# Performance work log

Measured on AMD Instinct MI355X. Metric: run time of the kernel, lower is better.

The kernel has to match this reference:

```python
import jax, jax.numpy as jnp
import numpy as np
from jax import lax

CIN, COUT = 128, 256
BN_EPS = 1e-5


def setup_inputs() -> dict:
    key = jax.random.key(0)
    ks = jax.random.split(key, 12)
    B, E, T = 4, 256, 128
    sc_in = 1.0 / np.sqrt(CIN)
    sc_out = 1.0 / np.sqrt(COUT)
    return {
        "x_e": jax.random.normal(ks[0], (B, E, T, CIN), dtype=jnp.float32),
        "Wp": jax.random.uniform(ks[1], (COUT, CIN), minval=-sc_in, maxval=sc_in, dtype=jnp.float32),
        "bp": jax.random.uniform(ks[2], (COUT,), minval=-sc_in, maxval=sc_in, dtype=jnp.float32),
        "a_param": jax.random.normal(ks[3], (COUT,), dtype=jnp.float32) * 0.1,
        "Wb": jax.random.uniform(ks[4], (COUT, COUT), minval=-sc_out, maxval=sc_out, dtype=jnp.float32),
        "bb": jax.random.uniform(ks[5], (COUT,), minval=-sc_out, maxval=sc_out, dtype=jnp.float32),
        "Wg": jax.random.uniform(ks[6], (COUT, COUT), minval=-sc_out, maxval=sc_out, dtype=jnp.float32),
        "bg": jax.random.uniform(ks[7], (COUT,), minval=-sc_out, maxval=sc_out, dtype=jnp.float32),
        "Wd": jax.random.uniform(ks[8], (COUT, COUT), minval=-sc_out, maxval=sc_out, dtype=jnp.float32),
        "bd": jax.random.uniform(ks[9], (COUT,), minval=-sc_out, maxval=sc_out, dtype=jnp.float32),
        "gamma": jnp.ones((COUT,), dtype=jnp.float32),
        "beta": jnp.zeros((COUT,), dtype=jnp.float32),
        "run_mean": jnp.zeros((COUT,), dtype=jnp.float32),
        "run_var": jnp.ones((COUT,), dtype=jnp.float32),
    }


def reference(x_e, Wp, bp, a_param, Wb, bb, Wg, bg, Wd, bd, gamma, beta, run_mean, run_var):
    # 1x1 conv over channel dim == pointwise linear: [B,E,T,Ci] @ [Co,Ci]^T
    x = jnp.einsum('betc,oc->beto', x_e, Wp) + bp              # [B,E,T,C]
    a = jnp.tanh(a_param)                                       # [C] per-channel decay
    u = jnp.einsum('betc,oc->beto', x, Wb) + bb                 # [B,E,T,C]

    # linear recurrence s_t = a * s_{t-1} + u_t, s_{-1} = 0 (scan over T)
    u_t = jnp.moveaxis(u, 2, 0)                                 # [T,B,E,C]

    def step(s, ut):
        s = a * s + ut
        return s, s

    s0 = jnp.zeros(u_t.shape[1:], dtype=u.dtype)
    _, S = lax.scan(step, s0, u_t)                              # [T,B,E,C]
    S = jnp.moveaxis(S, 0, 2)                                   # [B,E,T,C]

    # output projection applied to all timesteps at once
    y = (jnp.einsum('betc,oc->beto', S, Wg) + bg
         + jnp.einsum('betc,oc->beto', x, Wd) + bd)

    # BatchNorm2d (eval mode: running stats), channel-last layout
    y = (y - run_mean) * lax.rsqrt(run_var + BN_EPS) * gamma + beta
    y = jax.nn.gelu(y, approximate=False)
    return y + x  # dropout is identity in eval
```

## Files before the change

kernel.cpp:

```cpp
#include <hip/hip_runtime.h>
#include <hip/hip_bf16.h>

#define T 128
#define CIN 128
#define C 256
#define NBE 1024

typedef short bf8_t __attribute__((ext_vector_type(8)));
typedef float f4_t __attribute__((ext_vector_type(4)));

__device__ inline short f2bf(float f) {
  union { float f; unsigned u; } v; v.f = f;
  unsigned r = v.u + 0x7FFFu + ((v.u >> 16) & 1u);
  return (short)(r >> 16);
}
__device__ inline float bf2f(short s) {
  union { unsigned u; float f; } v; v.u = ((unsigned)(unsigned short)s) << 16;
  return v.f;
}
__device__ inline f4_t mfma16(bf8_t a, bf8_t b, f4_t c) {
  return __builtin_amdgcn_mfma_f32_16x16x32_bf16(a, b, c, 0, 0, 0);
}
__device__ inline bf8_t lds_frag(const short* base, int row, int kcol, int rowc) {
  return *reinterpret_cast<const bf8_t*>(base + row * rowc + (kcol ^ ((row & 7) << 3)));
}

__global__ void prep_weights(const float* __restrict__ Wp, const float* __restrict__ Wb,
                             const float* __restrict__ Wg, const float* __restrict__ Wd,
                             short* __restrict__ ws) {
  int i = blockIdx.x * 256 + threadIdx.x;
  if (i < 32768) ws[i] = f2bf(Wp[i]);
  ws[32768 + i]  = f2bf(Wb[i]);
  ws[98304 + i]  = f2bf(Wg[i]);
  ws[163840 + i] = f2bf(Wd[i]);
}

__global__ __launch_bounds__(512, 1) void fused_ssm(
    const float* __restrict__ xe, const short* __restrict__ wgt,
    const float* __restrict__ bp, const float* __restrict__ a_param,
    const float* __restrict__ bb, const float* __restrict__ bg,
    const float* __restrict__ bd, const float* __restrict__ gamma,
    const float* __restrict__ beta, const float* __restrict__ rmean,
    const float* __restrict__ rvar, float* __restrict__ out) {
  __shared__ __align__(16) short lds_x[T * C];
  __shared__ __align__(16) short lds_u[T * C];
  short* lds_xe = lds_u;

  const int tid = threadIdx.x;
  const int lane = tid & 63;
  const int w = tid >> 6;
  const int wr = w >> 1;
  const int wc = w & 1;
  const int l15 = lane & 15;
  const int l4 = lane >> 4;
  const int be = blockIdx.x;

  const float* xe_blk = xe + (size_t)be * T * CIN;
  float* out_blk = out + (size_t)be * T * C;

  const short* Wpb = wgt;
  const short* Wbb = wgt + 32768;
  const short* Wgb = wgt + 98304;
  const short* Wdb = wgt + 163840;

#pragma unroll
  for (int j = 0; j < 32; ++j) {
    int idx = j * 512 + tid;
    int r = idx >> 7, c = idx & 127;
    lds_xe[r * 128 + (c ^ ((r & 7) << 3))] = f2bf(xe_blk[idx]);
  }
  __syncthreads();

  const int row_a0 = wr * 32 + l15;
  const int col0 = wc * 128 + l15;

  f4_t acc[2][8];

#pragma unroll
  for (int mi = 0; mi < 2; ++mi)
#pragma unroll
    for (int ni = 0; ni < 8; ++ni) acc[mi][ni] = (f4_t)(0.f);

#pragma unroll
  for (int kk = 0; kk < 4; ++kk) {
    int kcol = kk * 32 + l4 * 8;
    bf8_t a0 = lds_frag(lds_xe, row_a0, kcol, 128);
    bf8_t a1 = lds_frag(lds_xe, row_a0 + 16, kcol, 128);
#pragma unroll
    for (int ni = 0; ni < 8; ++ni) {
      bf8_t b = *reinterpret_cast<const bf8_t*>(Wpb + (col0 + ni * 16) * 128 + kcol);
      acc[0][ni] = mfma16(a0, b, acc[0][ni]);
      acc[1][ni] = mfma16(a1, b, acc[1][ni]);
    }
  }
#pragma unroll
  for (int ni = 0; ni < 8; ++ni) {
    int col = col0 + ni * 16;
    float bias = bp[col];
#pragma unroll
    for (int mi = 0; mi < 2; ++mi)
#pragma unroll
      for (int r = 0; r < 4; ++r) {
        int row = wr * 32 + mi * 16 + l4 * 4 + r;
        lds_x[row * 256 + (col ^ ((row & 7) << 3))] = f2bf(acc[mi][ni][r] + bias);
      }
  }
  __syncthreads();

#pragma unroll
  for (int mi = 0; mi < 2; ++mi)
#pragma unroll
    for (int ni = 0; ni < 8; ++ni) acc[mi][ni] = (f4_t)(0.f);

#pragma unroll
  for (int kk = 0; kk < 8; ++kk) {
    int kcol = kk * 32 + l4 * 8;
    bf8_t a0 = lds_frag(lds_x, row_a0, kcol, 256);
    bf8_t a1 = lds_frag(lds_x, row_a0 + 16, kcol, 256);
#pragma unroll
    for (int ni = 0; ni < 8; ++ni) {
      bf8_t b = *reinterpret_cast<const bf8_t*>(Wbb + (col0 + ni * 16) * 256 + kcol);
      acc[0][ni] = mfma16(a0, b, acc[0][ni]);
      acc[1][ni] = mfma16(a1, b, acc[1][ni]);
    }
  }
#pragma unroll
  for (int ni = 0; ni < 8; ++ni) {
    int col = col0 + ni * 16;
    float bias = bb[col];
#pragma unroll
    for (int mi = 0; mi < 2; ++mi)
#pragma unroll
      for (int r = 0; r < 4; ++r) {
        int row = wr * 32 + mi * 16 + l4 * 4 + r;
        lds_u[row * 256 + (col ^ ((row & 7) << 3))] = f2bf(acc[mi][ni][r] + bias);
      }
  }
  __syncthreads();

  if (tid < 256) {
    float a = tanhf(a_param[tid]);
    float s = 0.f;
    for (int t = 0; t < T; ++t) {
      int idx = t * 256 + (tid ^ ((t & 7) << 3));
      s = a * s + bf2f(lds_u[idx]);
      lds_u[idx] = f2bf(s);
    }
  }
  __syncthreads();

#pragma unroll
  for (int mi = 0; mi < 2; ++mi)
#pragma unroll
    for (int ni = 0; ni < 8; ++ni) acc[mi][ni] = (f4_t)(0.f);

#pragma unroll
  for (int kk = 0; kk < 8; ++kk) {
    int kcol = kk * 32 + l4 * 8;
    bf8_t s0 = lds_frag(lds_u, row_a0, kcol, 256);
    bf8_t s1 = lds_frag(lds_u, row_a0 + 16, kcol, 256);
    bf8_t x0 = lds_frag(lds_x, row_a0, kcol, 256);
    bf8_t x1 = lds_frag(lds_x, row_a0 + 16, kcol, 256);
#pragma unroll
    for (int ni = 0; ni < 8; ++ni) {
      bf8_t bgf = *reinterpret_cast<const bf8_t*>(Wgb + (col0 + ni * 16) * 256 + kcol);
      acc[0][ni] = mfma16(s0, bgf, acc[0][ni]);
      acc[1][ni] = mfma16(s1, bgf, acc[1][ni]);
      bf8_t bdf = *reinterpret_cast<const bf8_t*>(Wdb + (col0 + ni * 16) * 256 + kcol);
      acc[0][ni] = mfma16(x0, bdf, acc[0][ni]);
      acc[1][ni] = mfma16(x1, bdf, acc[1][ni]);
    }
  }

#pragma unroll
  for (int ni = 0; ni < 8; ++ni) {
    int col = col0 + ni * 16;
    float bsum = bg[col] + bd[col];
    float mu = rmean[col];
    float rstd = rsqrtf(rvar[col] + 1e-5f);
    float ga = gamma[col], bt = beta[col];
#pragma unroll
    for (int mi = 0; mi < 2; ++mi)
#pragma unroll
      for (int r = 0; r < 4; ++r) {
        int row = wr * 32 + mi * 16 + l4 * 4 + r;
        float y = acc[mi][ni][r] + bsum;
        y = (y - mu) * rstd * ga + bt;
        float g = 0.5f * y * (1.f + erff(y * 0.70710678118654752f));
        float xv = bf2f(lds_x[row * 256 + (col ^ ((row & 7) << 3))]);
        out_blk[row * 256 + col] = g + xv;
      }
  }
}

extern "C" void kernel_launch(void* const* d_in, const int* in_sizes, int n_in,
                              void* d_out, int out_size, void* d_ws, size_t ws_size,
                              hipStream_t stream) {
  const float* xe    = (const float*)d_in[0];
  const float* Wp    = (const float*)d_in[1];
  const float* bp    = (const float*)d_in[2];
  const float* ap    = (const float*)d_in[3];
  const float* Wb    = (const float*)d_in[4];
  const float* bb    = (const float*)d_in[5];
  const float* Wg    = (const float*)d_in[6];
  const float* bg    = (const float*)d_in[7];
  const float* Wd    = (const float*)d_in[8];
  const float* bd    = (const float*)d_in[9];
  const float* gamma = (const float*)d_in[10];
  const float* beta  = (const float*)d_in[11];
  const float* rmean = (const float*)d_in[12];
  const float* rvar  = (const float*)d_in[13];
  float* out = (float*)d_out;
  short* wgt = (short*)d_ws;

  prep_weights<<<256, 256, 0, stream>>>(Wp, Wb, Wg, Wd, wgt);
  fused_ssm<<<NBE, 512, 0, stream>>>(xe, wgt, bp, ap, bb, bg, bd, gamma, beta,
                                     rmean, rvar, out);
}
```

Before: 298.0 us.

## Use 1024-thread blocks, vectorize input loads, and stage output through LDS

After: 376.4 us. +26.3%, slower.

```diff
diff --git a/kernel.cpp b/kernel.cpp
--- a/kernel.cpp
+++ b/kernel.cpp
@@ -7,6 +7,7 @@
 #define NBE 1024
 
 typedef short bf8_t __attribute__((ext_vector_type(8)));
+typedef short s4_t __attribute__((ext_vector_type(4)));
 typedef float f4_t __attribute__((ext_vector_type(4)));
 
 __device__ inline short f2bf(float f) {
@@ -35,22 +36,21 @@
   ws[163840 + i] = f2bf(Wd[i]);
 }
 
-__global__ __launch_bounds__(512, 1) void fused_ssm(
+__global__ __launch_bounds__(1024) void fused_ssm(
     const float* __restrict__ xe, const short* __restrict__ wgt,
     const float* __restrict__ bp, const float* __restrict__ a_param,
     const float* __restrict__ bb, const float* __restrict__ bg,
     const float* __restrict__ bd, const float* __restrict__ gamma,
     const float* __restrict__ beta, const float* __restrict__ rmean,
     const float* __restrict__ rvar, float* __restrict__ out) {
-  __shared__ __align__(16) short lds_x[T * C];
-  __shared__ __align__(16) short lds_u[T * C];
-  short* lds_xe = lds_u;
+  __shared__ __align__(16) short lds[2][T * C];
+  float* fbuf = reinterpret_cast<float*>(lds);
 
   const int tid = threadIdx.x;
   const int lane = tid & 63;
   const int w = tid >> 6;
-  const int wr = w >> 1;
-  const int wc = w & 1;
+  const int wr = w >> 2;
+  const int wcg = w & 3;
   const int l15 = lane & 15;
   const int l4 = lane >> 4;
   const int be = blockIdx.x;
@@ -63,46 +63,54 @@
   const short* Wgb = wgt + 98304;
   const short* Wdb = wgt + 163840;
 
-#pragma unroll
-  for (int j = 0; j < 32; ++j) {
-    int idx = j * 512 + tid;
-    int r = idx >> 7, c = idx & 127;
-    lds_xe[r * 128 + (c ^ ((r & 7) << 3))] = f2bf(xe_blk[idx]);
+  {
+    const float4* xe4 = reinterpret_cast<const float4*>(xe_blk);
+#pragma unroll
+    for (int j = 0; j < 4; ++j) {
+      float4 v = xe4[j * 1024 + tid];
+      int fi = j * 4096 + tid * 4;
+      int r = fi >> 7, c = fi & 127;
+      s4_t p = {f2bf(v.x), f2bf(v.y), f2bf(v.z), f2bf(v.w)};
+      *reinterpret_cast<s4_t*>(&lds[1][r * 128 + (c ^ ((r & 7) << 3))]) = p;
+    }
   }
   __syncthreads();
 
   const int row_a0 = wr * 32 + l15;
-  const int col0 = wc * 128 + l15;
-
-  f4_t acc[2][8];
+  const int colbase = wcg * 64 + l15;
+
+  f4_t acc[2][4];
 
 #pragma unroll
   for (int mi = 0; mi < 2; ++mi)
 #pragma unroll
-    for (int ni = 0; ni < 8; ++ni) acc[mi][ni] = (f4_t)(0.f);
+    for (int ni = 0; ni < 4; ++ni) acc[mi][ni] = (f4_t)(0.f);
 
 #pragma unroll
   for (int kk = 0; kk < 4; ++kk) {
     int kcol = kk * 32 + l4 * 8;
-    bf8_t a0 = lds_frag(lds_xe, row_a0, kcol, 128);
-    bf8_t a1 = lds_frag(lds_xe, row_a0 + 16, kcol, 128);
-#pragma unroll
-    for (int ni = 0; ni < 8; ++ni) {
-      bf8_t b = *reinterpret_cast<const bf8_t*>(Wpb + (col0 + ni * 16) * 128 + kcol);
-      acc[0][ni] = mfma16(a0, b, acc[0][ni]);
-      acc[1][ni] = mfma16(a1, b, acc[1][ni]);
-    }
-  }
-#pragma unroll
-  for (int ni = 0; ni < 8; ++ni) {
-    int col = col0 + ni * 16;
+    bf8_t a0 = lds_frag(lds[1], row_a0, kcol, 128);
+    bf8_t a1 = lds_frag(lds[1], row_a0 + 16, kcol, 128);
+    bf8_t bfr[4];
+#pragma unroll
+    for (int ni = 0; ni < 4; ++ni)
+      bfr[ni] = *reinterpret_cast<const bf8_t*>(Wpb + (colbase + ni * 16) * 128 + kcol);
+#pragma unroll
+    for (int ni = 0; ni < 4; ++ni) {
+      acc[0][ni] = mfma16(a0, bfr[ni], acc[0][ni]);
+      acc[1][ni] = mfma16(a1, bfr[ni], acc[1][ni]);
+    }
+  }
+#pragma unroll
+  for (int ni = 0; ni < 4; ++ni) {
+    int col = colbase + ni * 16;
     float bias = bp[col];
 #pragma unroll
     for (int mi = 0; mi < 2; ++mi)
 #pragma unroll
       for (int r = 0; r < 4; ++r) {
         int row = wr * 32 + mi * 16 + l4 * 4 + r;
-        lds_x[row * 256 + (col ^ ((row & 7) << 3))] = f2bf(acc[mi][ni][r] + bias);
+        lds[0][row * 256 + (col ^ ((row & 7) << 3))] = f2bf(acc[mi][ni][r] + bias);
       }
   }
   __syncthreads();
@@ -110,30 +118,33 @@
 #pragma unroll
   for (int mi = 0; mi < 2; ++mi)
 #pragma unroll
-    for (int ni = 0; ni < 8; ++ni) acc[mi][ni] = (f4_t)(0.f);
+    for (int ni = 0; ni < 4; ++ni) acc[mi][ni] = (f4_t)(0.f);
 
 #pragma unroll
   for (int kk = 0; kk < 8; ++kk) {
     int kcol = kk * 32 + l4 * 8;
-    bf8_t a0 = lds_frag(lds_x, row_a0, kcol, 256);
-    bf8_t a1 = lds_frag(lds_x, row_a0 + 16, kcol, 256);
-#pragma unroll
-    for (int ni = 0; ni < 8; ++ni) {
-      bf8_t b = *reinterpret_cast<const bf8_t*>(Wbb + (col0 + ni * 16) * 256 + kcol);
-      acc[0][ni] = mfma16(a0, b, acc[0][ni]);
-      acc[1][ni] = mfma16(a1, b, acc[1][ni]);
-    }
-  }
-#pragma unroll
-  for (int ni = 0; ni < 8; ++ni) {
-    int col = col0 + ni * 16;
+    bf8_t a0 = lds_frag(lds[0], row_a0, kcol, 256);
+    bf8_t a1 = lds_frag(lds[0], row_a0 + 16, kcol, 256);
+    bf8_t bfr[4];
+#pragma unroll
+    for (int ni = 0; ni < 4; ++ni)
+      bfr[ni] = *reinterpret_cast<const bf8_t*>(Wbb + (colbase + ni * 16) * 256 + kcol);
+#pragma unroll
+    for (int ni = 0; ni < 4; ++ni) {
+      acc[0][ni] = mfma16(a0, bfr[ni], acc[0][ni]);
+      acc[1][ni] = mfma16(a1, bfr[ni], acc[1][ni]);
+    }
+  }
+#pragma unroll
+  for (int ni = 0; ni < 4; ++ni) {
+    int col = colbase + ni * 16;
     float bias = bb[col];
 #pragma unroll
     for (int mi = 0; mi < 2; ++mi)
 #pragma unroll
       for (int r = 0; r < 4; ++r) {
         int row = wr * 32 + mi * 16 + l4 * 4 + r;
-        lds_u[row * 256 + (col ^ ((row & 7) << 3))] = f2bf(acc[mi][ni][r] + bias);
+        lds[1][row * 256 + (col ^ ((row & 7) << 3))] = f2bf(acc[mi][ni][r] + bias);
       }
   }
   __syncthreads();
@@ -141,10 +152,13 @@
   if (tid < 256) {
     float a = tanhf(a_param[tid]);
     float s = 0.f;
-    for (int t = 0; t < T; ++t) {
-      int idx = t * 256 + (tid ^ ((t & 7) << 3));
-      s = a * s + bf2f(lds_u[idx]);
-      lds_u[idx] = f2bf(s);
+    float un = bf2f(lds[1][tid]);
+#pragma unroll 8
+    for (int t = 0; t < 128; ++t) {
+      float unn = (t < 127) ? bf2f(lds[1][(t + 1) * 256 + (tid ^ (((t + 1) & 7) << 3))]) : 0.f;
+      s = a * s + un;
+      lds[1][t * 256 + (tid ^ ((t & 7) << 3))] = f2bf(s);
+      un = unn;
     }
   }
   __syncthreads();
@@ -152,29 +166,33 @@
 #pragma unroll
   for (int mi = 0; mi < 2; ++mi)
 #pragma unroll
-    for (int ni = 0; ni < 8; ++ni) acc[mi][ni] = (f4_t)(0.f);
+    for (int ni = 0; ni < 4; ++ni) acc[mi][ni] = (f4_t)(0.f);
 
 #pragma unroll
   for (int kk = 0; kk < 8; ++kk) {
     int kcol = kk * 32 + l4 * 8;
-    bf8_t s0 = lds_frag(lds_u, row_a0, kcol, 256);
-    bf8_t s1 = lds_frag(lds_u, row_a0 + 16, kcol, 256);
-    bf8_t x0 = lds_frag(lds_x, row_a0, kcol, 256);
-    bf8_t x1 = lds_frag(lds_x, row_a0 + 16, kcol, 256);
-#pragma unroll
-    for (int ni = 0; ni < 8; ++ni) {
-      bf8_t bgf = *reinterpret_cast<const bf8_t*>(Wgb + (col0 + ni * 16) * 256 + kcol);
-      acc[0][ni] = mfma16(s0, bgf, acc[0][ni]);
-      acc[1][ni] = mfma16(s1, bgf, acc[1][ni]);
-      bf8_t bdf = *reinterpret_cast<const bf8_t*>(Wdb + (col0 + ni * 16) * 256 + kcol);
-      acc[0][ni] = mfma16(x0, bdf, acc[0][ni]);
-      acc[1][ni] = mfma16(x1, bdf, acc[1][ni]);
-    }
-  }
-
-#pragma unroll
-  for (int ni = 0; ni < 8; ++ni) {
-    int col = col0 + ni * 16;
+    bf8_t s0 = lds_frag(lds[1], row_a0, kcol, 256);
+    bf8_t s1 = lds_frag(lds[1], row_a0 + 16, kcol, 256);
+    bf8_t x0 = lds_frag(lds[0], row_a0, kcol, 256);
+    bf8_t x1 = lds_frag(lds[0], row_a0 + 16, kcol, 256);
+    bf8_t bgf[4], bdf[4];
+#pragma unroll
+    for (int ni = 0; ni < 4; ++ni) {
+      bgf[ni] = *reinterpret_cast<const bf8_t*>(Wgb + (colbase + ni * 16) * 256 + kcol);
+      bdf[ni] = *reinterpret_cast<const bf8_t*>(Wdb + (colbase + ni * 16) * 256 + kcol);
+    }
+#pragma unroll
+    for (int ni = 0; ni < 4; ++ni) {
+      acc[0][ni] = mfma16(s0, bgf[ni], acc[0][ni]);
+      acc[1][ni] = mfma16(s1, bgf[ni], acc[1][ni]);
+      acc[0][ni] = mfma16(x0, bdf[ni], acc[0][ni]);
+      acc[1][ni] = mfma16(x1, bdf[ni], acc[1][ni]);
+    }
+  }
+
+#pragma unroll
+  for (int ni = 0; ni < 4; ++ni) {
+    int col = colbase + ni * 16;
     float bsum = bg[col] + bd[col];
     float mu = rmean[col];
     float rstd = rsqrtf(rvar[col] + 1e-5f);
@@ -187,9 +205,33 @@
         float y = acc[mi][ni][r] + bsum;
         y = (y - mu) * rstd * ga + bt;
         float g = 0.5f * y * (1.f + erff(y * 0.70710678118654752f));
-        float xv = bf2f(lds_x[row * 256 + (col ^ ((row & 7) << 3))]);
-        out_blk[row * 256 + col] = g + xv;
-      }
+        float xv = bf2f(lds[0][row * 256 + (col ^ ((row & 7) << 3))]);
+        acc[mi][ni][r] = g + xv;
+      }
+  }
+  __syncthreads();
+
+#pragma unroll
+  for (int ni = 0; ni < 4; ++ni) {
+    int col = colbase + ni * 16;
+#pragma unroll
+    for (int mi = 0; mi < 2; ++mi)
+#pragma unroll
+      for (int r = 0; r < 4; ++r) {
+        int row = wr * 32 + mi * 16 + l4 * 4 + r;
+        fbuf[row * 256 + (col ^ (l4 << 4))] = acc[mi][ni][r];
+      }
+  }
+  __syncthreads();
+
+  float4* out4 = reinterpret_cast<float4*>(out_blk);
+#pragma unroll
+  for (int j = 0; j < 8; ++j) {
+    int f4i = j * 1024 + tid;
+    int row = f4i >> 6;
+    int c4 = (f4i & 63) << 2;
+    int sc = c4 ^ (((row >> 2) & 3) << 4);
+    out4[f4i] = *reinterpret_cast<float4*>(&fbuf[row * 256 + sc]);
   }
 }
 
@@ -214,6 +256,6 @@
   short* wgt = (short*)d_ws;
 
   prep_weights<<<256, 256, 0, stream>>>(Wp, Wb, Wg, Wd, wgt);
-  fused_ssm<<<NBE, 512, 0, stream>>>(xe, wgt, bp, ap, bb, bg, bd, gamma, beta,
-                                     rmean, rvar, out);
-}
+  fused_ssm<<<NBE, 1024, 0, stream>>>(xe, wgt, bp, ap, bb, bg, bd, gamma, beta,
+                                      rmean, rvar, out);
+}
```

## Split fused SSM kernel into projection, scan, and output kernels via workspace

Applied to the files above, without the earlier changes.

New measurement: 400.1 us. +34.3%, slower.

```diff
diff --git a/kernel.cpp b/kernel.cpp
--- a/kernel.cpp
+++ b/kernel.cpp
@@ -5,8 +5,10 @@
 #define CIN 128
 #define C 256
 #define NBE 1024
+#define MROWS (NBE * T)
 
 typedef short bf8_t __attribute__((ext_vector_type(8)));
+typedef short s4_t __attribute__((ext_vector_type(4)));
 typedef float f4_t __attribute__((ext_vector_type(4)));
 
 __device__ inline short f2bf(float f) {
@@ -35,7 +37,246 @@
   ws[163840 + i] = f2bf(Wd[i]);
 }
 
-__global__ __launch_bounds__(512, 1) void fused_ssm(
+__global__ __launch_bounds__(256, 1) void k1_proj(
+    const float* __restrict__ xe, const short* __restrict__ wgt,
+    const float* __restrict__ bp, const float* __restrict__ bb,
+    short* __restrict__ xg, short* __restrict__ uS) {
+  __shared__ __align__(16) short xe_s[64 * 128];
+  __shared__ __align__(16) short x_s[64 * 256];
+
+  const int tid = threadIdx.x;
+  const int lane = tid & 63;
+  const int w = tid >> 6;
+  const int wr = w >> 1;
+  const int wcg = w & 1;
+  const int l15 = lane & 15;
+  const int l4 = lane >> 4;
+  const int row0 = blockIdx.x * 64;
+
+  const short* Wpb = wgt;
+  const short* Wbb = wgt + 32768;
+
+  {
+    const float4* xe4 = reinterpret_cast<const float4*>(xe + (size_t)row0 * CIN);
+#pragma unroll
+    for (int j = 0; j < 8; ++j) {
+      float4 v = xe4[j * 256 + tid];
+      int fi = (j * 256 + tid) * 4;
+      int r = fi >> 7, c = fi & 127;
+      s4_t p = {f2bf(v.x), f2bf(v.y), f2bf(v.z), f2bf(v.w)};
+      *reinterpret_cast<s4_t*>(&xe_s[r * 128 + (c ^ ((r & 7) << 3))]) = p;
+    }
+  }
+  __syncthreads();
+
+  const int row_a0 = wr * 32 + l15;
+  const int colbase = wcg * 128 + l15;
+
+  f4_t acc[2][8];
+#pragma unroll
+  for (int mi = 0; mi < 2; ++mi)
+#pragma unroll
+    for (int ni = 0; ni < 8; ++ni) acc[mi][ni] = (f4_t)(0.f);
+
+#pragma unroll
+  for (int kk = 0; kk < 4; ++kk) {
+    int kcol = kk * 32 + l4 * 8;
+    bf8_t a0 = lds_frag(xe_s, row_a0, kcol, 128);
+    bf8_t a1 = lds_frag(xe_s, row_a0 + 16, kcol, 128);
+#pragma unroll
+    for (int ni = 0; ni < 8; ++ni) {
+      bf8_t b = *reinterpret_cast<const bf8_t*>(Wpb + (colbase + ni * 16) * 128 + kcol);
+      acc[0][ni] = mfma16(a0, b, acc[0][ni]);
+      acc[1][ni] = mfma16(a1, b, acc[1][ni]);
+    }
+  }
+#pragma unroll
+  for (int ni = 0; ni < 8; ++ni) {
+    int col = colbase + ni * 16;
+    float bias = bp[col];
+#pragma unroll
+    for (int mi = 0; mi < 2; ++mi)
+#pragma unroll
+      for (int r = 0; r < 4; ++r) {
+        int row = wr * 32 + mi * 16 + l4 * 4 + r;
+        x_s[row * 256 + (col ^ ((row & 7) << 3))] = f2bf(acc[mi][ni][r] + bias);
+      }
+  }
+  __syncthreads();
+
+#pragma unroll
+  for (int mi = 0; mi < 2; ++mi)
+#pragma unroll
+    for (int ni = 0; ni < 8; ++ni) acc[mi][ni] = (f4_t)(0.f);
+#pragma unroll
+  for (int kk = 0; kk < 8; ++kk) {
+    int kcol = kk * 32 + l4 * 8;
+    bf8_t a0 = lds_frag(x_s, row_a0, kcol, 256);
+    bf8_t a1 = lds_frag(x_s, row_a0 + 16, kcol, 256);
+#pragma unroll
+    for (int ni = 0; ni < 8; ++ni) {
+      bf8_t b = *reinterpret_cast<const bf8_t*>(Wbb + (colbase + ni * 16) * 256 + kcol);
+      acc[0][ni] = mfma16(a0, b, acc[0][ni]);
+      acc[1][ni] = mfma16(a1, b, acc[1][ni]);
+    }
+  }
+#pragma unroll
+  for (int j = 0; j < 8; ++j) {
+    int chunk = j * 256 + tid;
+    int r = chunk >> 5, c8 = chunk & 31;
+    bf8_t v = *reinterpret_cast<const bf8_t*>(&x_s[r * 256 + ((c8 * 8) ^ ((r & 7) << 3))]);
+    *reinterpret_cast<bf8_t*>(&xg[(size_t)(row0 + r) * 256 + c8 * 8]) = v;
+  }
+  __syncthreads();
+
+#pragma unroll
+  for (int ni = 0; ni < 8; ++ni) {
+    int col = colbase + ni * 16;
+    float bias = bb[col];
+#pragma unroll
+    for (int mi = 0; mi < 2; ++mi)
+#pragma unroll
+      for (int r = 0; r < 4; ++r) {
+        int row = wr * 32 + mi * 16 + l4 * 4 + r;
+        x_s[row * 256 + (col ^ ((row & 7) << 3))] = f2bf(acc[mi][ni][r] + bias);
+      }
+  }
+  __syncthreads();
+#pragma unroll
+  for (int j = 0; j < 8; ++j) {
+    int chunk = j * 256 + tid;
+    int r = chunk >> 5, c8 = chunk & 31;
+    bf8_t v = *reinterpret_cast<const bf8_t*>(&x_s[r * 256 + ((c8 * 8) ^ ((r & 7) << 3))]);
+    *reinterpret_cast<bf8_t*>(&uS[(size_t)(row0 + r) * 256 + c8 * 8]) = v;
+  }
+}
+
+__global__ __launch_bounds__(256, 1) void k2_scan(
+    const float* __restrict__ ap, short* __restrict__ uS) {
+  const int be = blockIdx.x;
+  const int c = threadIdx.x;
+  short* p = uS + (size_t)be * T * C + c;
+  float a = tanhf(ap[c]);
+  float un[4];
+#pragma unroll
+  for (int j = 0; j < 4; ++j) un[j] = bf2f(p[j * C]);
+  float s = 0.f;
+#pragma unroll 4
+  for (int t = 0; t < T; ++t) {
+    float nx = (t + 4 < T) ? bf2f(p[(t + 4) * C]) : 0.f;
+    s = a * s + un[0];
+    p[t * C] = f2bf(s);
+    un[0] = un[1]; un[1] = un[2]; un[2] = un[3]; un[3] = nx;
+  }
+}
+
+__global__ __launch_bounds__(256, 1) void k3_out(
+    const short* __restrict__ wgt, const short* __restrict__ xg,
+    const short* __restrict__ uS, const float* __restrict__ bg,
+    const float* __restrict__ bd, const float* __restrict__ gamma,
+    const float* __restrict__ beta, const float* __restrict__ rmean,
+    const float* __restrict__ rvar, float* __restrict__ out) {
+  __shared__ __align__(16) short lds2[2][64 * 256];
+  float* fbuf = reinterpret_cast<float*>(lds2);
+
+  const int tid = threadIdx.x;
+  const int lane = tid & 63;
+  const int w = tid >> 6;
+  const int wr = w >> 1;
+  const int wcg = w & 1;
+  const int l15 = lane & 15;
+  const int l4 = lane >> 4;
+  const int row0 = blockIdx.x * 64;
+
+  const short* Wgb = wgt + 98304;
+  const short* Wdb = wgt + 163840;
+
+#pragma unroll
+  for (int j = 0; j < 8; ++j) {
+    int chunk = j * 256 + tid;
+    int r = chunk >> 5, c8 = chunk & 31;
+    int loff = r * 256 + ((c8 * 8) ^ ((r & 7) << 3));
+    size_t goff = (size_t)(row0 + r) * 256 + c8 * 8;
+    *reinterpret_cast<bf8_t*>(&lds2[0][loff]) =
+        *reinterpret_cast<const bf8_t*>(&uS[goff]);
+    *reinterpret_cast<bf8_t*>(&lds2[1][loff]) =
+        *reinterpret_cast<const bf8_t*>(&xg[goff]);
+  }
+  __syncthreads();
+
+  const int row_a0 = wr * 32 + l15;
+  const int colbase = wcg * 128 + l15;
+
+  f4_t acc[2][8];
+#pragma unroll
+  for (int mi = 0; mi < 2; ++mi)
+#pragma unroll
+    for (int ni = 0; ni < 8; ++ni) acc[mi][ni] = (f4_t)(0.f);
+
+#pragma unroll
+  for (int kk = 0; kk < 8; ++kk) {
+    int kcol = kk * 32 + l4 * 8;
+    bf8_t s0 = lds_frag(lds2[0], row_a0, kcol, 256);
+    bf8_t s1 = lds_frag(lds2[0], row_a0 + 16, kcol, 256);
+    bf8_t x0 = lds_frag(lds2[1], row_a0, kcol, 256);
+    bf8_t x1 = lds_frag(lds2[1], row_a0 + 16, kcol, 256);
+#pragma unroll
+    for (int ni = 0; ni < 8; ++ni) {
+      bf8_t bgf = *reinterpret_cast<const bf8_t*>(Wgb + (colbase + ni * 16) * 256 + kcol);
+      acc[0][ni] = mfma16(s0, bgf, acc[0][ni]);
+      acc[1][ni] = mfma16(s1, bgf, acc[1][ni]);
+      bf8_t bdf = *reinterpret_cast<const bf8_t*>(Wdb + (colbase + ni * 16) * 256 + kcol);
+      acc[0][ni] = mfma16(x0, bdf, acc[0][ni]);
+      acc[1][ni] = mfma16(x1, bdf, acc[1][ni]);
+    }
+  }
+
+#pragma unroll
+  for (int ni = 0; ni < 8; ++ni) {
+    int col = colbase + ni * 16;
+    float bsum = bg[col] + bd[col];
+    float mu = rmean[col];
+    float rstd = rsqrtf(rvar[col] + 1e-5f);
+    float ga = gamma[col], bt = beta[col];
+#pragma unroll
+    for (int mi = 0; mi < 2; ++mi)
+#pragma unroll
+      for (int r = 0; r < 4; ++r) {
+        int row = wr * 32 + mi * 16 + l4 * 4 + r;
+        float y = acc[mi][ni][r] + bsum;
+        y = (y - mu) * rstd * ga + bt;
+        float g = 0.5f * y * (1.f + erff(y * 0.70710678118654752f));
+        float xv = bf2f(lds2[1][row * 256 + (col ^ ((row & 7) << 3))]);
+        acc[mi][ni][r] = g + xv;
+      }
+  }
+  __syncthreads();
+
+#pragma unroll
+  for (int ni = 0; ni < 8; ++ni) {
+    int col = colbase + ni * 16;
+#pragma unroll
+    for (int mi = 0; mi < 2; ++mi)
+#pragma unroll
+      for (int r = 0; r < 4; ++r) {
+        int row = wr * 32 + mi * 16 + l4 * 4 + r;
+        fbuf[row * 256 + (col ^ (l4 << 4))] = acc[mi][ni][r];
+      }
+  }
+  __syncthreads();
+
+  float4* out4 = reinterpret_cast<float4*>(out + (size_t)row0 * 256);
+#pragma unroll
+  for (int j = 0; j < 16; ++j) {
+    int f4i = j * 256 + tid;
+    int row = f4i >> 6;
+    int c4 = (f4i & 63) << 2;
+    int sc = c4 ^ (((row >> 2) & 3) << 4);
+    out4[f4i] = *reinterpret_cast<float4*>(&fbuf[row * 256 + sc]);
+  }
+}
+
+__global__ __launch_bounds__(512, 1) void fused_fallback(
     const float* __restrict__ xe, const short* __restrict__ wgt,
     const float* __restrict__ bp, const float* __restrict__ a_param,
     const float* __restrict__ bb, const float* __restrict__ bg,
@@ -73,14 +314,12 @@
 
   const int row_a0 = wr * 32 + l15;
   const int col0 = wc * 128 + l15;
-
   f4_t acc[2][8];
 
 #pragma unroll
   for (int mi = 0; mi < 2; ++mi)
 #pragma unroll
     for (int ni = 0; ni < 8; ++ni) acc[mi][ni] = (f4_t)(0.f);
-
 #pragma unroll
   for (int kk = 0; kk < 4; ++kk) {
     int kcol = kk * 32 + l4 * 8;
@@ -111,7 +350,6 @@
   for (int mi = 0; mi < 2; ++mi)
 #pragma unroll
     for (int ni = 0; ni < 8; ++ni) acc[mi][ni] = (f4_t)(0.f);
-
 #pragma unroll
   for (int kk = 0; kk < 8; ++kk) {
     int kcol = kk * 32 + l4 * 8;
@@ -141,19 +379,21 @@
   if (tid < 256) {
     float a = tanhf(a_param[tid]);
     float s = 0.f;
-    for (int t = 0; t < T; ++t) {
-      int idx = t * 256 + (tid ^ ((t & 7) << 3));
-      s = a * s + bf2f(lds_u[idx]);
-      lds_u[idx] = f2bf(s);
-    }
-  }
-  __syncthreads();
-
-#pragma unroll
-  for (int mi = 0; mi < 2; ++mi)
-#pragma unroll
-    for (int ni = 0; ni < 8; ++ni) acc[mi][ni] = (f4_t)(0.f);
-
+    float un = bf2f(lds_u[tid]);
+#pragma unroll 8
+    for (int t = 0; t < 128; ++t) {
+      float unn = (t < 127) ? bf2f(lds_u[(t + 1) * 256 + (tid ^ (((t + 1) & 7) << 3))]) : 0.f;
+      s = a * s + un;
+      lds_u[t * 256 + (tid ^ ((t & 7) << 3))] = f2bf(s);
+      un = unn;
+    }
+  }
+  __syncthreads();
+
+#pragma unroll
+  for (int mi = 0; mi < 2; ++mi)
+#pragma unroll
+    for (int ni = 0; ni < 8; ++ni) acc[mi][ni] = (f4_t)(0.f);
 #pragma unroll
   for (int kk = 0; kk < 8; ++kk) {
     int kcol = kk * 32 + l4 * 8;
@@ -211,9 +451,23 @@
   const float* rmean = (const float*)d_in[12];
   const float* rvar  = (const float*)d_in[13];
   float* out = (float*)d_out;
+
   short* wgt = (short*)d_ws;
+  const size_t XG_OFF = 458752;
+  const size_t US_OFF = XG_OFF + (size_t)MROWS * C * 2;
+  const size_t NEED = US_OFF + (size_t)MROWS * C * 2;
 
   prep_weights<<<256, 256, 0, stream>>>(Wp, Wb, Wg, Wd, wgt);
-  fused_ssm<<<NBE, 512, 0, stream>>>(xe, wgt, bp, ap, bb, bg, bd, gamma, beta,
-                                     rmean, rvar, out);
-}
+
+  if (ws_size >= NEED) {
+    short* xg = (short*)((char*)d_ws + XG_OFF);
+    short* uS = (short*)((char*)d_ws + US_OFF);
+    k1_proj<<<MROWS / 64, 256, 0, stream>>>(xe, wgt, bp, bb, xg, uS);
+    k2_scan<<<NBE, 256, 0, stream>>>(ap, uS);
+    k3_out<<<MROWS / 64, 256, 0, stream>>>(wgt, xg, uS, bg, bd, gamma, beta,
+                                           rmean, rvar, out);
+  } else {
+    fused_fallback<<<NBE, 512, 0, stream>>>(xe, wgt, bp, ap, bb, bg, bd, gamma,
+                                            beta, rmean, rvar, out);
+  }
+}
```
